# Performance work log

Hardware: AMD Instinct MI355X
Metric: run time of the kernel (lower is better)

## Reference

```python
import jax, jax.numpy as jnp
import numpy as np

N_NODES = 50000
N_EDGES = 800000
IN_C, HID_C, OUT_C = 64, 128, 40


def setup_inputs() -> dict:
    key = jax.random.key(0)
    ks = jax.random.split(key, 8)
    x = jax.random.normal(ks[0], (N_NODES, IN_C), dtype=jnp.float32)
    edge_index = jax.random.randint(ks[1], (2, N_EDGES), 0, N_NODES, dtype=jnp.int64)
    def lin(k, fan_in, fan_out):
        # torch Linear default init: U(-1/sqrt(fan_in), 1/sqrt(fan_in))
        bound = 1.0 / np.sqrt(fan_in)
        kw, kb = jax.random.split(k)
        w = jax.random.uniform(kw, (fan_in, fan_out), minval=-bound, maxval=bound, dtype=jnp.float32)
        b = jax.random.uniform(kb, (fan_out,), minval=-bound, maxval=bound, dtype=jnp.float32)
        return w, b
    w1a, b1a = lin(ks[2], IN_C, HID_C)
    w1b, b1b = lin(ks[3], HID_C, HID_C)
    w2a, b2a = lin(ks[4], HID_C, HID_C)
    w2b, b2b = lin(ks[5], HID_C, OUT_C)
    return {
        'x': x, 'edge_index': edge_index,
        'w1a': w1a, 'b1a': b1a, 'w1b': w1b, 'b1b': b1b, 'eps1': jnp.float32(0.0),
        'w2a': w2a, 'b2a': b2a, 'w2b': w2b, 'b2b': b2b, 'eps2': jnp.float32(0.0),
    }


def _gin_conv(x, src, dst, eps, wa, ba, wb, bb):
    # aggregate: sum of neighbor (source) features at each destination node
    agg = jax.ops.segment_sum(x[src], dst, num_segments=N_NODES)  # [N, d]
    h = (1.0 + eps) * x + agg
    h = jax.nn.relu(h @ wa + ba)
    return h @ wb + bb


def reference(x, edge_index, w1a, b1a, w1b, b1b, eps1, w2a, b2a, w2b, b2b, eps2):
    src, dst = edge_index[0], edge_index[1]
    h = _gin_conv(x, src, dst, eps1, w1a, b1a, w1b, b1b)
    h = jax.nn.relu(h)
    # F.dropout(training=False) -> identity at inference
    h = _gin_conv(h, src, dst, eps2, w2a, b2a, w2b, b2b)
    return jax.nn.log_softmax(h, axis=1)
```

## Files before the change

### kernel.cpp

```cpp
#include <hip/hip_runtime.h>
#include <math.h>

#define N_NODES 50000
#define N_EDGES 800000
#define DUMMY   50000

typedef __attribute__((ext_vector_type(4))) _Float16 half4;
typedef __attribute__((ext_vector_type(8))) _Float16 half8;
typedef __attribute__((ext_vector_type(4))) float f32x4;

#define F_W1A 0
#define F_W1B (16 * 128)
#define F_W2A (48 * 128)
#define F_W2B (80 * 128)

__global__ __launch_bounds__(256) void prep(const float4* __restrict__ in,
    half4* __restrict__ xh4, int* __restrict__ zbase, half4* __restrict__ h1dummy,
    const float* __restrict__ w1a, const float* __restrict__ w1b,
    const float* __restrict__ w2a, const float* __restrict__ w2b,
    half8* __restrict__ wfrag)
{
    int i = blockIdx.x * 256 + threadIdx.x;
    if (i < 450000) zbase[i] = 0;
    if (i < 800000) {
        float4 v = in[i];
        half4 h;
        h[0] = (_Float16)v.x; h[1] = (_Float16)v.y;
        h[2] = (_Float16)v.z; h[3] = (_Float16)v.w;
        xh4[i] = h;
    } else if (i < 800016) {
        half4 zer = {(_Float16)0.f, (_Float16)0.f, (_Float16)0.f, (_Float16)0.f};
        xh4[i] = zer;
    }
    if (i < 32) {
        half4 zer = {(_Float16)0.f, (_Float16)0.f, (_Float16)0.f, (_Float16)0.f};
        h1dummy[i] = zer;
    }
    int j = i - 800032;
    if (j >= 0 && j < 5888) {
        int l = j & 63, f = j >> 6;
        const float* W; int fi, s, ct, Nw, base;
        if (f < 16)      { W = w1a; fi = f;      s = fi >> 3; ct = fi & 7;    Nw = 128; base = F_W1A; }
        else if (f < 48) { W = w1b; fi = f - 16; s = fi >> 3; ct = fi & 7;    Nw = 128; base = F_W1B; }
        else if (f < 80) { W = w2a; fi = f - 48; s = fi >> 3; ct = fi & 7;    Nw = 128; base = F_W2A; }
        else             { W = w2b; fi = f - 80; s = fi / 3;  ct = fi - s*3;  Nw = 40;  base = F_W2B; }
        int c = ct * 16 + (l & 15);
        int k0 = s * 32 + (l >> 4) * 8;
        half8 hi, lo;
        #pragma unroll
        for (int t = 0; t < 8; ++t) {
            float wv = (c < Nw) ? W[(k0 + t) * Nw + c] : 0.0f;
            _Float16 h = (_Float16)wv;
            hi[t] = h;
            lo[t] = (_Float16)(wv - (float)h);
        }
        wfrag[base + (fi * 2 + 0) * 64 + l] = hi;
        wfrag[base + (fi * 2 + 1) * 64 + l] = lo;
    }
}

__global__ __launch_bounds__(256) void scatter_ell(const int* __restrict__ src,
    const int* __restrict__ dst, int* __restrict__ cursor8, int* __restrict__ ovcur,
    unsigned short* __restrict__ ellp, unsigned short* __restrict__ ovell)
{
    int g = blockIdx.x & 7;
    int el = (blockIdx.x >> 3) * 256 + threadIdx.x;
    if (el >= 100000) return;
    int e = g * 100000 + el;
    int d = dst[e];
    unsigned short s = (unsigned short)src[e];
    int slot = atomicAdd(&cursor8[g * 50000 + d], 1);
    if (slot < 8) ellp[(size_t)(g * 50000 + d) * 8 + slot] = s;
    else {
        int o = atomicAdd(&ovcur[d], 1);
        if (o < 16) ovell[d * 16 + o] = s;
    }
}

__global__ __launch_bounds__(256) void gather64c(const half8* __restrict__ rows,
    const int* __restrict__ cursor8, const int* __restrict__ ovcur,
    const unsigned short* __restrict__ ellp, const unsigned short* __restrict__ ovell,
    unsigned short* __restrict__ ell, int* __restrict__ deg,
    const float* __restrict__ epsp, half8* __restrict__ z)
{
    __shared__ unsigned short buf[4][80];
    const float eps = 1.0f + epsp[0];
    const int lane = threadIdx.x & 63;
    const int w = threadIdx.x >> 6;
    const int q = lane & 7, p = lane >> 3;
    const int sl = lane & 7;
    const int wid = blockIdx.x * 4 + w;
    const int wstep = gridDim.x * 4;

    for (int node = wid; node < N_NODES; node += wstep) {
        int cg = min(cursor8[p * 50000 + node], 8);
        bool valid = sl < cg;
        unsigned short v = ellp[(size_t)(p * 50000 + node) * 8 + sl];
        unsigned long long mask = __ballot(valid);
        int total = __popcll(mask);
        int pos = __popcll(mask & ((1ULL << lane) - 1ULL));
        if (valid) buf[w][pos] = v;
        int ov = min(ovcur[node], 16);
        if (lane < ov) buf[w][total + lane] = ovell[node * 16 + lane];
        int tot = min(total + ov, 64);
        unsigned short e = (lane < tot) ? buf[w][lane] : (unsigned short)DUMMY;
        ell[((size_t)node << 6) + lane] = e;
        if (lane == 0) deg[node] = tot;
        int eidx = e;
        float acc[8];
        #pragma unroll
        for (int j = 0; j < 8; ++j) acc[j] = 0.f;
        for (int i = 0; i < tot; i += 32) {
            int s0 = __shfl(eidx, i + p);
            int s1 = __shfl(eidx, i + 8 + p);
            int s2 = __shfl(eidx, i + 16 + p);
            int s3 = __shfl(eidx, i + 24 + p);
            half8 v0 = rows[s0 * 8 + q];
            half8 v1 = rows[s1 * 8 + q];
            half8 v2 = rows[s2 * 8 + q];
            half8 v3 = rows[s3 * 8 + q];
            #pragma unroll
            for (int j = 0; j < 8; ++j)
                acc[j] += ((float)v0[j] + (float)v1[j]) + ((float)v2[j] + (float)v3[j]);
        }
        #pragma unroll
        for (int j = 0; j < 8; ++j) {
            acc[j] += __shfl_xor(acc[j], 8);
            acc[j] += __shfl_xor(acc[j], 16);
            acc[j] += __shfl_xor(acc[j], 32);
        }
        if (p == 0) {
            half8 sv = rows[node * 8 + q];
            half8 o;
            #pragma unroll
            for (int j = 0; j < 8; ++j) o[j] = (_Float16)fmaf(eps, (float)sv[j], acc[j]);
            z[node * 8 + q] = o;
        }
    }
}

__global__ __launch_bounds__(256) void gather128(const half8* __restrict__ rows,
    const unsigned short* __restrict__ ell, const int* __restrict__ deg,
    const float* __restrict__ epsp, half8* __restrict__ z)
{
    const float eps = 1.0f + epsp[0];
    const int lane = threadIdx.x & 63;
    const int q = lane & 15, p = lane >> 4;
    const int wid = blockIdx.x * 4 + (threadIdx.x >> 6);
    const int wstep = gridDim.x * 4;

    for (int node = wid; node < N_NODES; node += wstep) {
        const int cnt = deg[node];
        int eidx = ell[((size_t)node << 6) + lane];
        float acc[8];
        #pragma unroll
        for (int j = 0; j < 8; ++j) acc[j] = 0.f;
        for (int i = 0; i < cnt; i += 16) {
            int s0 = __shfl(eidx, i + p);
            int s1 = __shfl(eidx, i + 4 + p);
            int s2 = __shfl(eidx, i + 8 + p);
            int s3 = __shfl(eidx, i + 12 + p);
            half8 v0 = rows[s0 * 16 + q];
            half8 v1 = rows[s1 * 16 + q];
            half8 v2 = rows[s2 * 16 + q];
            half8 v3 = rows[s3 * 16 + q];
            #pragma unroll
            for (int j = 0; j < 8; ++j)
                acc[j] += ((float)v0[j] + (float)v1[j]) + ((float)v2[j] + (float)v3[j]);
        }
        #pragma unroll
        for (int j = 0; j < 8; ++j) {
            acc[j] += __shfl_xor(acc[j], 16);
            acc[j] += __shfl_xor(acc[j], 32);
        }
        if (p == 0) {
            half8 sv = rows[node * 16 + q];
            half8 o;
            #pragma unroll
            for (int j = 0; j < 8; ++j) o[j] = (_Float16)fmaf(eps, (float)sv[j], acc[j]);
            z[node * 16 + q] = o;
        }
    }
}

template<int KA, int NB, int EPI>
__global__ __launch_bounds__(256) void fused_mlp(const _Float16* __restrict__ A,
    const half8* __restrict__ wAF, const float* __restrict__ bA,
    const half8* __restrict__ wBF, const float* __restrict__ bB,
    void* __restrict__ Cout)
{
    constexpr int SA = KA / 32, CTB = NB / 16;
    __shared__ char mid[4][4096];
    const int tid = threadIdx.x;
    const int lane = tid & 63;
    const int wave = tid >> 6;
    const int gg = lane >> 4, r16 = lane & 15;
    const int tile = blockIdx.x * 4 + wave;
    if (tile >= (N_NODES + 15) / 16) return;
    char* my = mid[wave];

    const _Float16* Ar = A + (size_t)(tile * 16 + r16) * KA;
    f32x4 acc[8];
    #pragma unroll
    for (int ct = 0; ct < 8; ++ct) acc[ct] = (f32x4){0.f, 0.f, 0.f, 0.f};
    #pragma unroll
    for (int s = 0; s < SA; ++s) {
        half8 a = *(const half8*)(Ar + s * 32 + gg * 8);
        #pragma unroll
        for (int ct = 0; ct < 8; ++ct) {
            half8 bh = wAF[((s * 8 + ct) * 2 + 0) * 64 + lane];
            half8 bo = wAF[((s * 8 + ct) * 2 + 1) * 64 + lane];
            acc[ct] = __builtin_amdgcn_mfma_f32_16x16x32_f16(a, bh, acc[ct], 0, 0, 0);
            acc[ct] = __builtin_amdgcn_mfma_f32_16x16x32_f16(a, bo, acc[ct], 0, 0, 0);
        }
    }
    #pragma unroll
    for (int ct = 0; ct < 8; ++ct) {
        float bb = bA[ct * 16 + r16];
        #pragma unroll
        for (int r = 0; r < 4; ++r) {
            int row = gg * 4 + r;
            float v = fmaxf(acc[ct][r] + bb, 0.0f);
            int off = (row << 8) + ((ct * 16 + r16) << 1);
            off ^= (row & 7) << 4;
            *(_Float16*)(my + off) = (_Float16)v;
        }
    }

    half8 a2[4];
    #pragma unroll
    for (int s = 0; s < 4; ++s) {
        int off = (r16 << 8) + (s << 6) + (gg << 4);
        off ^= (r16 & 7) << 4;
        a2[s] = *(const half8*)(my + off);
    }
    f32x4 acc2[CTB];
    #pragma unroll
    for (int ct = 0; ct < CTB; ++ct) acc2[ct] = (f32x4){0.f, 0.f, 0.f, 0.f};
    #pragma unroll
    for (int s = 0; s < 4; ++s) {
        #pragma unroll
        for (int ct = 0; ct < CTB; ++ct) {
            half8 bh = wBF[((s * CTB + ct) * 2 + 0) * 64 + lane];
            half8 bo = wBF[((s * CTB + ct) * 2 + 1) * 64 + lane];
            acc2[ct] = __builtin_amdgcn_mfma_f32_16x16x32_f16(a2[s], bh, acc2[ct], 0, 0, 0);
            acc2[ct] = __builtin_amdgcn_mfma_f32_16x16x32_f16(a2[s], bo, acc2[ct], 0, 0, 0);
        }
    }

    if (EPI == 0) {
        _Float16* C = (_Float16*)Cout;
        #pragma unroll
        for (int ct = 0; ct < CTB; ++ct) {
            float bb = bB[ct * 16 + r16];
            #pragma unroll
            for (int r = 0; r < 4; ++r) {
                int row = tile * 16 + gg * 4 + r;
                float v = fmaxf(acc2[ct][r] + bb, 0.0f);
                C[(size_t)row * NB + ct * 16 + r16] = (_Float16)v;
            }
        }
    } else {
        float* C = (float*)Cout;
        const bool va2 = r16 < 8;
        float bl0 = bB[r16], bl1 = bB[16 + r16];
        float bl2 = va2 ? bB[32 + r16] : 0.0f;
        #pragma unroll
        for (int r = 0; r < 4; ++r) {
            int row = tile * 16 + gg * 4 + r;
            float v0 = acc2[0][r] + bl0;
            float v1 = acc2[1][r] + bl1;
            float v2 = acc2[2][r] + bl2;
            float mx = fmaxf(fmaxf(v0, v1), va2 ? v2 : -__builtin_inff());
            mx = fmaxf(mx, __shfl_xor(mx, 1));
            mx = fmaxf(mx, __shfl_xor(mx, 2));
            mx = fmaxf(mx, __shfl_xor(mx, 4));
            mx = fmaxf(mx, __shfl_xor(mx, 8));
            float sm = expf(v0 - mx) + expf(v1 - mx) + (va2 ? expf(v2 - mx) : 0.f);
            sm += __shfl_xor(sm, 1);
            sm += __shfl_xor(sm, 2);
            sm += __shfl_xor(sm, 4);
            sm += __shfl_xor(sm, 8);
            float ls = logf(sm) + mx;
            C[row * 40 + r16] = v0 - ls;
            C[row * 40 + 16 + r16] = v1 - ls;
            if (va2) C[row * 40 + 32 + r16] = v2 - ls;
        }
    }
}

extern "C" void kernel_launch(void* const* d_in, const int* in_sizes, int n_in,
                              void* d_out, int out_size, void* d_ws, size_t ws_size,
                              hipStream_t stream) {
    const float* x    = (const float*)d_in[0];
    const int*   ei   = (const int*)d_in[1];
    const float* w1a  = (const float*)d_in[2];
    const float* b1a  = (const float*)d_in[3];
    const float* w1b  = (const float*)d_in[4];
    const float* b1b  = (const float*)d_in[5];
    const float* eps1 = (const float*)d_in[6];
    const float* w2a  = (const float*)d_in[7];
    const float* b2a  = (const float*)d_in[8];
    const float* w2b  = (const float*)d_in[9];
    const float* b2b  = (const float*)d_in[10];
    const float* eps2 = (const float*)d_in[11];
    float* out = (float*)d_out;

    const int* srcIdx = ei;
    const int* dstIdx = ei + N_EDGES;

    char* ws = (char*)d_ws;
    int*            cursor8 = (int*)(ws);
    int*            ovcur   = (int*)(ws + 1600000);
    unsigned short* ellp    = (unsigned short*)(ws + 1800000);
    unsigned short* ovell   = (unsigned short*)(ws + 8200000);
    unsigned short* ell     = (unsigned short*)(ws + 9800000);
    int*            deg     = (int*)(ws + 16200000);
    half8*          wfrag   = (half8*)(ws + 16400000);
    _Float16*       xh      = (_Float16*)(ws + 16600000);
    _Float16*       z1h     = (_Float16*)(ws + 23000192);
    _Float16*       h1h     = (_Float16*)(ws + 29400192);
    _Float16*       z2h     = (_Float16*)(ws + 42200448);
    half4*          h1dummy = (half4*)(h1h + (size_t)DUMMY * 128);

    prep<<<3149, 256, 0, stream>>>((const float4*)x, (half4*)xh, cursor8, h1dummy,
                                   w1a, w1b, w2a, w2b, wfrag);
    scatter_ell<<<3128, 256, 0, stream>>>(srcIdx, dstIdx, cursor8, ovcur, ellp, ovell);

    gather64c<<<2048, 256, 0, stream>>>((const half8*)xh, cursor8, ovcur, ellp, ovell,
                                        ell, deg, eps1, (half8*)z1h);
    fused_mlp<64, 128, 0><<<782, 256, 0, stream>>>(z1h, wfrag + F_W1A, b1a,
                                                   wfrag + F_W1B, b1b, h1h);
    gather128<<<2048, 256, 0, stream>>>((const half8*)h1h, ell, deg, eps2, (half8*)z2h);
    fused_mlp<128, 48, 1><<<782, 256, 0, stream>>>(z2h, wfrag + F_W2A, b2a,
                                                   wfrag + F_W2B, b2b, out);
}
```

Measured before the change: 212.1 us.

## Merge prep and scatter kernels, split gathers across column groups with fixed 64-edge loads

Counter zeroing moves to a memset, and the prep and scatter kernels are merged into one launch with block ranges picking the role. The two gather kernels are restructured so that blockIdx.y selects a column group: 2 groups for the 64-wide layer and 4 for the 128-wide layer. Each wave now loads all 64 ELL slots, with padding pointing at a zeroed dummy row, in one unrolled step instead of looping over the degree. This raises parallelism and removes the dependent loop, but it re-reads the edge lists per column group and always loads 64 neighbours even for low-degree nodes. The merged prep_scatter kernel relies on the memset finishing before any atomics, which stream order guarantees.

```diff
diff --git a/kernel.cpp b/kernel.cpp
--- a/kernel.cpp
+++ b/kernel.cpp
@@ -14,14 +14,34 @@
 #define F_W2A (48 * 128)
 #define F_W2B (80 * 128)
 
-__global__ __launch_bounds__(256) void prep(const float4* __restrict__ in,
-    half4* __restrict__ xh4, int* __restrict__ zbase, half4* __restrict__ h1dummy,
+#define SCATTER_BLOCKS 3128
+#define PREP_BLOCKS    3149
+
+__global__ __launch_bounds__(256) void prep_scatter(
+    const int* __restrict__ src, const int* __restrict__ dst,
+    int* __restrict__ cursor8, int* __restrict__ ovcur,
+    unsigned short* __restrict__ ellp, unsigned short* __restrict__ ovell,
+    const float4* __restrict__ in, half4* __restrict__ xh4, half4* __restrict__ h1dummy,
     const float* __restrict__ w1a, const float* __restrict__ w1b,
     const float* __restrict__ w2a, const float* __restrict__ w2b,
     half8* __restrict__ wfrag)
 {
-    int i = blockIdx.x * 256 + threadIdx.x;
-    if (i < 450000) zbase[i] = 0;
+    if (blockIdx.x < SCATTER_BLOCKS) {
+        int g = blockIdx.x & 7;
+        int el = (blockIdx.x >> 3) * 256 + threadIdx.x;
+        if (el >= 100000) return;
+        int e = g * 100000 + el;
+        int d = dst[e];
+        unsigned short s = (unsigned short)src[e];
+        int slot = atomicAdd(&cursor8[g * 50000 + d], 1);
+        if (slot < 8) ellp[(size_t)(g * 50000 + d) * 8 + slot] = s;
+        else {
+            int o = atomicAdd(&ovcur[d], 1);
+            if (o < 16) ovell[d * 16 + o] = s;
+        }
+        return;
+    }
+    int i = (blockIdx.x - SCATTER_BLOCKS) * 256 + threadIdx.x;
     if (i < 800000) {
         float4 v = in[i];
         half4 h;
@@ -59,24 +79,6 @@
     }
 }
 
-__global__ __launch_bounds__(256) void scatter_ell(const int* __restrict__ src,
-    const int* __restrict__ dst, int* __restrict__ cursor8, int* __restrict__ ovcur,
-    unsigned short* __restrict__ ellp, unsigned short* __restrict__ ovell)
-{
-    int g = blockIdx.x & 7;
-    int el = (blockIdx.x >> 3) * 256 + threadIdx.x;
-    if (el >= 100000) return;
-    int e = g * 100000 + el;
-    int d = dst[e];
-    unsigned short s = (unsigned short)src[e];
-    int slot = atomicAdd(&cursor8[g * 50000 + d], 1);
-    if (slot < 8) ellp[(size_t)(g * 50000 + d) * 8 + slot] = s;
-    else {
-        int o = atomicAdd(&ovcur[d], 1);
-        if (o < 16) ovell[d * 16 + o] = s;
-    }
-}
-
 __global__ __launch_bounds__(256) void gather64c(const half8* __restrict__ rows,
     const int* __restrict__ cursor8, const int* __restrict__ ovcur,
     const unsigned short* __restrict__ ellp, const unsigned short* __restrict__ ovell,
@@ -85,17 +87,18 @@
 {
     __shared__ unsigned short buf[4][80];
     const float eps = 1.0f + epsp[0];
+    const int cg = blockIdx.y;
     const int lane = threadIdx.x & 63;
     const int w = threadIdx.x >> 6;
-    const int q = lane & 7, p = lane >> 3;
-    const int sl = lane & 7;
+    const int q = lane & 3, p = lane >> 2;
+    const int gpl = lane >> 3, sl = lane & 7;
     const int wid = blockIdx.x * 4 + w;
     const int wstep = gridDim.x * 4;
 
     for (int node = wid; node < N_NODES; node += wstep) {
-        int cg = min(cursor8[p * 50000 + node], 8);
-        bool valid = sl < cg;
-        unsigned short v = ellp[(size_t)(p * 50000 + node) * 8 + sl];
+        int cgn = min(cursor8[gpl * 50000 + node], 8);
+        bool valid = sl < cgn;
+        unsigned short v = ellp[(size_t)(gpl * 50000 + node) * 8 + sl];
         unsigned long long mask = __ballot(valid);
         int total = __popcll(mask);
         int pos = __popcll(mask & ((1ULL << lane) - 1ULL));
@@ -104,81 +107,80 @@
         if (lane < ov) buf[w][total + lane] = ovell[node * 16 + lane];
         int tot = min(total + ov, 64);
         unsigned short e = (lane < tot) ? buf[w][lane] : (unsigned short)DUMMY;
-        ell[((size_t)node << 6) + lane] = e;
-        if (lane == 0) deg[node] = tot;
+        if (cg == 0) {
+            ell[((size_t)node << 6) + lane] = e;
+            if (lane == 0) deg[node] = tot;
+        }
         int eidx = e;
+        int s0 = __shfl(eidx, p);
+        int s1 = __shfl(eidx, 16 + p);
+        int s2 = __shfl(eidx, 32 + p);
+        int s3 = __shfl(eidx, 48 + p);
+        int base = cg * 4 + q;
+        half8 v0 = rows[s0 * 8 + base];
+        half8 v1 = rows[s1 * 8 + base];
+        half8 v2 = rows[s2 * 8 + base];
+        half8 v3 = rows[s3 * 8 + base];
         float acc[8];
         #pragma unroll
-        for (int j = 0; j < 8; ++j) acc[j] = 0.f;
-        for (int i = 0; i < tot; i += 32) {
-            int s0 = __shfl(eidx, i + p);
-            int s1 = __shfl(eidx, i + 8 + p);
-            int s2 = __shfl(eidx, i + 16 + p);
-            int s3 = __shfl(eidx, i + 24 + p);
-            half8 v0 = rows[s0 * 8 + q];
-            half8 v1 = rows[s1 * 8 + q];
-            half8 v2 = rows[s2 * 8 + q];
-            half8 v3 = rows[s3 * 8 + q];
-            #pragma unroll
-            for (int j = 0; j < 8; ++j)
-                acc[j] += ((float)v0[j] + (float)v1[j]) + ((float)v2[j] + (float)v3[j]);
-        }
+        for (int j = 0; j < 8; ++j)
+            acc[j] = ((float)v0[j] + (float)v1[j]) + ((float)v2[j] + (float)v3[j]);
         #pragma unroll
         for (int j = 0; j < 8; ++j) {
+            acc[j] += __shfl_xor(acc[j], 4);
             acc[j] += __shfl_xor(acc[j], 8);
             acc[j] += __shfl_xor(acc[j], 16);
             acc[j] += __shfl_xor(acc[j], 32);
         }
         if (p == 0) {
-            half8 sv = rows[node * 8 + q];
+            half8 sv = rows[node * 8 + base];
             half8 o;
             #pragma unroll
             for (int j = 0; j < 8; ++j) o[j] = (_Float16)fmaf(eps, (float)sv[j], acc[j]);
-            z[node * 8 + q] = o;
+            z[node * 8 + base] = o;
         }
     }
 }
 
 __global__ __launch_bounds__(256) void gather128(const half8* __restrict__ rows,
-    const unsigned short* __restrict__ ell, const int* __restrict__ deg,
+    const unsigned short* __restrict__ ell,
     const float* __restrict__ epsp, half8* __restrict__ z)
 {
     const float eps = 1.0f + epsp[0];
+    const int cg = blockIdx.y;
     const int lane = threadIdx.x & 63;
-    const int q = lane & 15, p = lane >> 4;
+    const int q = lane & 3, p = lane >> 2;
     const int wid = blockIdx.x * 4 + (threadIdx.x >> 6);
     const int wstep = gridDim.x * 4;
 
     for (int node = wid; node < N_NODES; node += wstep) {
-        const int cnt = deg[node];
         int eidx = ell[((size_t)node << 6) + lane];
+        int s0 = __shfl(eidx, p);
+        int s1 = __shfl(eidx, 16 + p);
+        int s2 = __shfl(eidx, 32 + p);
+        int s3 = __shfl(eidx, 48 + p);
+        int base = cg * 4 + q;
+        half8 v0 = rows[s0 * 16 + base];
+        half8 v1 = rows[s1 * 16 + base];
+        half8 v2 = rows[s2 * 16 + base];
+        half8 v3 = rows[s3 * 16 + base];
         float acc[8];
         #pragma unroll
-        for (int j = 0; j < 8; ++j) acc[j] = 0.f;
-        for (int i = 0; i < cnt; i += 16) {
-            int s0 = __shfl(eidx, i + p);
-            int s1 = __shfl(eidx, i + 4 + p);
-            int s2 = __shfl(eidx, i + 8 + p);
-            int s3 = __shfl(eidx, i + 12 + p);
-            half8 v0 = rows[s0 * 16 + q];
-            half8 v1 = rows[s1 * 16 + q];
-            half8 v2 = rows[s2 * 16 + q];
-            half8 v3 = rows[s3 * 16 + q];
-            #pragma unroll
-            for (int j = 0; j < 8; ++j)
-                acc[j] += ((float)v0[j] + (float)v1[j]) + ((float)v2[j] + (float)v3[j]);
-        }
+        for (int j = 0; j < 8; ++j)
+            acc[j] = ((float)v0[j] + (float)v1[j]) + ((float)v2[j] + (float)v3[j]);
         #pragma unroll
         for (int j = 0; j < 8; ++j) {
+            acc[j] += __shfl_xor(acc[j], 4);
+            acc[j] += __shfl_xor(acc[j], 8);
             acc[j] += __shfl_xor(acc[j], 16);
             acc[j] += __shfl_xor(acc[j], 32);
         }
         if (p == 0) {
-            half8 sv = rows[node * 16 + q];
+            half8 sv = rows[node * 16 + base];
             half8 o;
             #pragma unroll
             for (int j = 0; j < 8; ++j) o[j] = (_Float16)fmaf(eps, (float)sv[j], acc[j]);
-            z[node * 16 + q] = o;
+            z[node * 16 + base] = o;
         }
     }
 }
@@ -323,15 +325,17 @@
     _Float16*       z2h     = (_Float16*)(ws + 42200448);
     half4*          h1dummy = (half4*)(h1h + (size_t)DUMMY * 128);
 
-    prep<<<3149, 256, 0, stream>>>((const float4*)x, (half4*)xh, cursor8, h1dummy,
-                                   w1a, w1b, w2a, w2b, wfrag);
-    scatter_ell<<<3128, 256, 0, stream>>>(srcIdx, dstIdx, cursor8, ovcur, ellp, ovell);
-
-    gather64c<<<2048, 256, 0, stream>>>((const half8*)xh, cursor8, ovcur, ellp, ovell,
-                                        ell, deg, eps1, (half8*)z1h);
+    hipMemsetAsync(cursor8, 0, 1800000, stream);
+
+    prep_scatter<<<SCATTER_BLOCKS + PREP_BLOCKS, 256, 0, stream>>>(
+        srcIdx, dstIdx, cursor8, ovcur, ellp, ovell,
+        (const float4*)x, (half4*)xh, h1dummy, w1a, w1b, w2a, w2b, wfrag);
+
+    gather64c<<<dim3(1024, 2), 256, 0, stream>>>((const half8*)xh, cursor8, ovcur,
+                                                 ellp, ovell, ell, deg, eps1, (half8*)z1h);
     fused_mlp<64, 128, 0><<<782, 256, 0, stream>>>(z1h, wfrag + F_W1A, b1a,
                                                    wfrag + F_W1B, b1b, h1h);
-    gather128<<<2048, 256, 0, stream>>>((const half8*)h1h, ell, deg, eps2, (half8*)z2h);
+    gather128<<<dim3(1024, 4), 256, 0, stream>>>((const half8*)h1h, ell, eps2, (half8*)z2h);
     fused_mlp<128, 48, 1><<<782, 256, 0, stream>>>(z2h, wfrag + F_W2A, b2a,
                                                    wfrag + F_W2B, b2b, out);
 }
```

Measured after the change: 297.0 us. +40.1%, slower.
